# Kernel tuning notes

Hardware: AMD Instinct MI355X
Metric: run time of the kernel (lower is better)

## Reference

```python
import jax, jax.numpy as jnp
import numpy as np

B, N, D, CDIM = 32, 100000, 3, 128


def setup_inputs() -> dict:
    key = jax.random.key(0)
    ks = jax.random.split(key, 24)
    def lin(kw, kb, out_dim, in_dim):
        s = 1.0 / np.sqrt(in_dim)
        W = jax.random.uniform(kw, (out_dim, in_dim), jnp.float32, -s, s)
        b = jax.random.uniform(kb, (out_dim,), jnp.float32, -s, s)
        return W, b
    inp = {}
    inp["t"] = jnp.zeros((1,), jnp.float32)
    inp["x"] = jax.random.normal(ks[0], (B, N, D), jnp.float32)
    inp["c"] = jax.random.normal(ks[1], (B, CDIM), jnp.float32)
    i = 2
    for tag in ("0", "1", "2"):
        W, b = lin(ks[i], ks[i + 1], D, D); i += 2
        Ws, bs = lin(ks[i], ks[i + 1], D, CDIM); i += 2
        Wb, bb = lin(ks[i], ks[i + 1], D, CDIM); i += 2
        inp["W" + tag], inp["b" + tag] = W, b
        inp["Ws" + tag], inp["bs" + tag] = Ws, bs
        inp["Wb" + tag], inp["bb" + tag] = Wb, bb
    return inp


def _block(x, c, W, b, Ws, bs, Wb, bb):
    # FiLM-conditioned linear: fc(x) * sigmoid(fc_scale(c)) + fc_bias(c)
    scale = jax.nn.sigmoid(c @ Ws.T + bs)[:, None, :]  # [B,1,D]
    bias = (c @ Wb.T + bb)[:, None, :]                  # [B,1,D]
    return (x @ W.T + b) * scale + bias                 # [B,N,D]


def reference(t, x, c,
              W0, b0, Ws0, bs0, Wb0, bb0,
              W1, b1, Ws1, bs1, Wb1, bb1,
              W2, b2, Ws2, bs2, Wb2, bb2):
    h = jnp.tanh(_block(x, c, W0, b0, Ws0, bs0, Wb0, bb0))
    h = jnp.tanh(_block(h, c, W1, b1, Ws1, bs1, Wb1, bb1))
    # last four blocks share the fc_2 / fc_scale_2 / fc_bias_2 weights
    for _ in range(4):
        h = jnp.tanh(_block(h, c, W2, b2, Ws2, bs2, Wb2, bb2))
    return h
```

## Files before the change

### kernel.cpp

```cpp
#include <hip/hip_runtime.h>
#include <math.h>

#define NBATCH 32
#define NPTS   100000
#define CD     128
#define PPT    8

#define C2LOG2E 2.8853900817779268f

#if defined(__has_builtin)
#if __has_builtin(__builtin_amdgcn_exp2f)
#define FAST_EXP2(v) __builtin_amdgcn_exp2f(v)
#endif
#endif
#ifndef FAST_EXP2
#define FAST_EXP2(v) __expf((v) * 0.6931471805599453f)
#endif

__device__ __forceinline__ float tanh_pre(float yp) {
    yp = fminf(fmaxf(yp, -30.0f), 30.0f);
    float e = FAST_EXP2(yp);
    float r = __builtin_amdgcn_rcpf(e + 1.0f);
    return fmaf(-2.0f, r, 1.0f);
}

__global__ void film_params_kernel(
    const float* __restrict__ c,
    const float* __restrict__ W0, const float* __restrict__ b0,
    const float* __restrict__ Ws0, const float* __restrict__ bs0,
    const float* __restrict__ Wb0, const float* __restrict__ bb0,
    const float* __restrict__ W1, const float* __restrict__ b1,
    const float* __restrict__ Ws1, const float* __restrict__ bs1,
    const float* __restrict__ Wb1, const float* __restrict__ bb1,
    const float* __restrict__ W2, const float* __restrict__ b2,
    const float* __restrict__ Ws2, const float* __restrict__ bs2,
    const float* __restrict__ Wb2, const float* __restrict__ bb2,
    float* __restrict__ params)
{
    int idx = blockIdx.x * blockDim.x + threadIdx.x;
    if (idx >= NBATCH * 3 * 3) return;
    int d   = idx % 3;
    int tag = (idx / 3) % 3;
    int b   = idx / 9;

    const float* Wt[3]  = {W0, W1, W2};
    const float* bt[3]  = {b0, b1, b2};
    const float* Wst[3] = {Ws0, Ws1, Ws2};
    const float* bst[3] = {bs0, bs1, bs2};
    const float* Wbt[3] = {Wb0, Wb1, Wb2};
    const float* bbt[3] = {bb0, bb1, bb2};

    const float* crow  = c + b * CD;
    const float* wsrow = Wst[tag] + d * CD;
    const float* wbrow = Wbt[tag] + d * CD;
    float sacc = bst[tag][d];
    float bacc = bbt[tag][d];
    for (int k = 0; k < CD; ++k) {
        float cv = crow[k];
        sacc = fmaf(cv, wsrow[k], sacc);
        bacc = fmaf(cv, wbrow[k], bacc);
    }
    float scale = 1.0f / (1.0f + expf(-sacc));
    float cs = C2LOG2E * scale;

    float* o = params + (b * 3 + tag) * 12;
    o[d * 3 + 0] = cs * Wt[tag][d * 3 + 0];
    o[d * 3 + 1] = cs * Wt[tag][d * 3 + 1];
    o[d * 3 + 2] = cs * Wt[tag][d * 3 + 2];
    o[9 + d]     = C2LOG2E * (bt[tag][d] * scale + bacc);
}

__global__ __launch_bounds__(256) void film_main_kernel(
    const float* __restrict__ x, const float* __restrict__ params,
    float* __restrict__ out, int nthreads)
{
    int t = blockIdx.x * blockDim.x + threadIdx.x;
    if (t >= nthreads) return;
    int p0 = t * PPT;
    int b  = p0 / NPTS;

    const float* P = params + b * 36;
    float M0[9], M1[9], M2[9], v0[3], v1[3], v2[3];
#pragma unroll
    for (int i = 0; i < 9; ++i) { M0[i] = P[i]; M1[i] = P[12 + i]; M2[i] = P[24 + i]; }
#pragma unroll
    for (int i = 0; i < 3; ++i) { v0[i] = P[9 + i]; v1[i] = P[21 + i]; v2[i] = P[33 + i]; }

    float a[3 * PPT];
    const float4* xin = (const float4*)(x + (size_t)p0 * 3);
#pragma unroll
    for (int i = 0; i < (3 * PPT) / 4; ++i) ((float4*)a)[i] = xin[i];

#define APPLY(M, v)                                                       \
    {                                                                     \
        float y0 = fmaf(M[0], h0, fmaf(M[1], h1, fmaf(M[2], h2, v[0]))); \
        float y1 = fmaf(M[3], h0, fmaf(M[4], h1, fmaf(M[5], h2, v[1]))); \
        float y2 = fmaf(M[6], h0, fmaf(M[7], h1, fmaf(M[8], h2, v[2]))); \
        h0 = tanh_pre(y0); h1 = tanh_pre(y1); h2 = tanh_pre(y2);         \
    }

#pragma unroll
    for (int p = 0; p < PPT; ++p) {
        float h0 = a[p * 3 + 0], h1 = a[p * 3 + 1], h2 = a[p * 3 + 2];
        APPLY(M0, v0);
        APPLY(M1, v1);
#pragma unroll
        for (int r = 0; r < 4; ++r) { APPLY(M2, v2); }
        a[p * 3 + 0] = h0; a[p * 3 + 1] = h1; a[p * 3 + 2] = h2;
    }
#undef APPLY

    float4* op = (float4*)(out + (size_t)p0 * 3);
#pragma unroll
    for (int i = 0; i < (3 * PPT) / 4; ++i) op[i] = ((float4*)a)[i];
}

extern "C" void kernel_launch(void* const* d_in, const int* in_sizes, int n_in,
                              void* d_out, int out_size, void* d_ws, size_t ws_size,
                              hipStream_t stream)
{
    const float* x = (const float*)d_in[1];
    const float* c = (const float*)d_in[2];
    float* params = (float*)d_ws;

    film_params_kernel<<<dim3(5), dim3(64), 0, stream>>>(
        c,
        (const float*)d_in[3],  (const float*)d_in[4],  (const float*)d_in[5],
        (const float*)d_in[6],  (const float*)d_in[7],  (const float*)d_in[8],
        (const float*)d_in[9],  (const float*)d_in[10], (const float*)d_in[11],
        (const float*)d_in[12], (const float*)d_in[13], (const float*)d_in[14],
        (const float*)d_in[15], (const float*)d_in[16], (const float*)d_in[17],
        (const float*)d_in[18], (const float*)d_in[19], (const float*)d_in[20],
        params);

    int nthreads = (NBATCH * NPTS) / PPT;
    int grid = (nthreads + 255) / 256;
    film_main_kernel<<<dim3(grid), dim3(256), 0, stream>>>(
        x, params, (float*)d_out, nthreads);
}
```

Measured before the change: 150.1 us.

## Fuse FiLM parameter computation into main kernel with per-batch block mapping

```diff
diff --git a/kernel.cpp b/kernel.cpp
--- a/kernel.cpp
+++ b/kernel.cpp
@@ -5,27 +5,21 @@
 #define NPTS   100000
 #define CD     128
 #define PPT    8
+#define TPB    256
+#define THREADS_PER_BATCH (NPTS / PPT)
+#define BLKS_PER_BATCH 49
 
 #define C2LOG2E 2.8853900817779268f
-
-#if defined(__has_builtin)
-#if __has_builtin(__builtin_amdgcn_exp2f)
-#define FAST_EXP2(v) __builtin_amdgcn_exp2f(v)
-#endif
-#endif
-#ifndef FAST_EXP2
-#define FAST_EXP2(v) __expf((v) * 0.6931471805599453f)
-#endif
+#define LOG2E   1.4426950408889634f
 
 __device__ __forceinline__ float tanh_pre(float yp) {
-    yp = fminf(fmaxf(yp, -30.0f), 30.0f);
-    float e = FAST_EXP2(yp);
+    float e = __builtin_amdgcn_exp2f(yp);
     float r = __builtin_amdgcn_rcpf(e + 1.0f);
     return fmaf(-2.0f, r, 1.0f);
 }
 
-__global__ void film_params_kernel(
-    const float* __restrict__ c,
+__global__ __launch_bounds__(TPB) void film_fused_kernel(
+    const float* __restrict__ x, const float* __restrict__ c,
     const float* __restrict__ W0, const float* __restrict__ b0,
     const float* __restrict__ Ws0, const float* __restrict__ bs0,
     const float* __restrict__ Wb0, const float* __restrict__ bb0,
@@ -35,59 +29,88 @@
     const float* __restrict__ W2, const float* __restrict__ b2,
     const float* __restrict__ Ws2, const float* __restrict__ bs2,
     const float* __restrict__ Wb2, const float* __restrict__ bb2,
-    float* __restrict__ params)
+    float* __restrict__ out)
 {
-    int idx = blockIdx.x * blockDim.x + threadIdx.x;
-    if (idx >= NBATCH * 3 * 3) return;
-    int d   = idx % 3;
-    int tag = (idx / 3) % 3;
-    int b   = idx / 9;
+    __shared__ float lds_part[18][8];
+    __shared__ float lds_red[18];
+    __shared__ float lds_params[36];
 
-    const float* Wt[3]  = {W0, W1, W2};
-    const float* bt[3]  = {b0, b1, b2};
-    const float* Wst[3] = {Ws0, Ws1, Ws2};
-    const float* bst[3] = {bs0, bs1, bs2};
-    const float* Wbt[3] = {Wb0, Wb1, Wb2};
-    const float* bbt[3] = {bb0, bb1, bb2};
+    const int tid = threadIdx.x;
+    const int blk = blockIdx.x;
+    const int b = blk / BLKS_PER_BATCH;
+    const int blk_in_b = blk - b * BLKS_PER_BATCH;
 
-    const float* crow  = c + b * CD;
-    const float* wsrow = Wst[tag] + d * CD;
-    const float* wbrow = Wbt[tag] + d * CD;
-    float sacc = bst[tag][d];
-    float bacc = bbt[tag][d];
-    for (int k = 0; k < CD; ++k) {
-        float cv = crow[k];
-        sacc = fmaf(cv, wsrow[k], sacc);
-        bacc = fmaf(cv, wbrow[k], bacc);
+    if (tid < 144) {
+        const int g = tid >> 3, j = tid & 7;
+        const int tag = g / 6;
+        const int r = g - tag * 6;
+        const int d = r >> 1, which = r & 1;
+        const float* Wsel;
+        if (tag == 0)      Wsel = which ? Wb0 : Ws0;
+        else if (tag == 1) Wsel = which ? Wb1 : Ws1;
+        else               Wsel = which ? Wb2 : Ws2;
+        const float4* row4 = (const float4*)(Wsel + d * CD);
+        const float4* c4   = (const float4*)(c + b * CD);
+        float acc = 0.0f;
+#pragma unroll
+        for (int i = 0; i < 4; ++i) {
+            float4 cv = c4[j * 4 + i];
+            float4 wv = row4[j * 4 + i];
+            acc = fmaf(cv.x, wv.x, acc);
+            acc = fmaf(cv.y, wv.y, acc);
+            acc = fmaf(cv.z, wv.z, acc);
+            acc = fmaf(cv.w, wv.w, acc);
+        }
+        lds_part[g][j] = acc;
     }
-    float scale = 1.0f / (1.0f + expf(-sacc));
-    float cs = C2LOG2E * scale;
+    __syncthreads();
+    if (tid < 18) {
+        float s = 0.0f;
+#pragma unroll
+        for (int j = 0; j < 8; ++j) s += lds_part[tid][j];
+        lds_red[tid] = s;
+    }
+    __syncthreads();
+    if (tid < 9) {
+        const int tag = tid / 3, d = tid - tag * 3;
+        const float *Wt, *bt, *bst, *bbt;
+        if (tag == 0)      { Wt = W0; bt = b0; bst = bs0; bbt = bb0; }
+        else if (tag == 1) { Wt = W1; bt = b1; bst = bs1; bbt = bb1; }
+        else               { Wt = W2; bt = b2; bst = bs2; bbt = bb2; }
+        float sacc = lds_red[tag * 6 + d * 2 + 0] + bst[d];
+        float bacc = lds_red[tag * 6 + d * 2 + 1] + bbt[d];
+        float scale = 1.0f / (1.0f + __builtin_amdgcn_exp2f(-sacc * LOG2E));
+        float cs = C2LOG2E * scale;
+        float* o = lds_params + tag * 12;
+        o[d * 3 + 0] = cs * Wt[d * 3 + 0];
+        o[d * 3 + 1] = cs * Wt[d * 3 + 1];
+        o[d * 3 + 2] = cs * Wt[d * 3 + 2];
+        o[9 + d]     = C2LOG2E * fmaf(bt[d], scale, bacc);
+    }
+    __syncthreads();
 
-    float* o = params + (b * 3 + tag) * 12;
-    o[d * 3 + 0] = cs * Wt[tag][d * 3 + 0];
-    o[d * 3 + 1] = cs * Wt[tag][d * 3 + 1];
-    o[d * 3 + 2] = cs * Wt[tag][d * 3 + 2];
-    o[9 + d]     = C2LOG2E * (bt[tag][d] * scale + bacc);
-}
+    float M0[9], M1[9], M2[9], v0[3], v1[3], v2[3];
+    {
+        const float4* P = (const float4*)lds_params;
+        float4 q;
+        q = P[0]; M0[0]=q.x; M0[1]=q.y; M0[2]=q.z; M0[3]=q.w;
+        q = P[1]; M0[4]=q.x; M0[5]=q.y; M0[6]=q.z; M0[7]=q.w;
+        q = P[2]; M0[8]=q.x; v0[0]=q.y; v0[1]=q.z; v0[2]=q.w;
+        q = P[3]; M1[0]=q.x; M1[1]=q.y; M1[2]=q.z; M1[3]=q.w;
+        q = P[4]; M1[4]=q.x; M1[5]=q.y; M1[6]=q.z; M1[7]=q.w;
+        q = P[5]; M1[8]=q.x; v1[0]=q.y; v1[1]=q.z; v1[2]=q.w;
+        q = P[6]; M2[0]=q.x; M2[1]=q.y; M2[2]=q.z; M2[3]=q.w;
+        q = P[7]; M2[4]=q.x; M2[5]=q.y; M2[6]=q.z; M2[7]=q.w;
+        q = P[8]; M2[8]=q.x; v2[0]=q.y; v2[1]=q.z; v2[2]=q.w;
+    }
 
-__global__ __launch_bounds__(256) void film_main_kernel(
-    const float* __restrict__ x, const float* __restrict__ params,
-    float* __restrict__ out, int nthreads)
-{
-    int t = blockIdx.x * blockDim.x + threadIdx.x;
-    if (t >= nthreads) return;
-    int p0 = t * PPT;
-    int b  = p0 / NPTS;
+    const int t_local = blk_in_b * TPB + tid;
+    if (t_local >= THREADS_PER_BATCH) return;
 
-    const float* P = params + b * 36;
-    float M0[9], M1[9], M2[9], v0[3], v1[3], v2[3];
-#pragma unroll
-    for (int i = 0; i < 9; ++i) { M0[i] = P[i]; M1[i] = P[12 + i]; M2[i] = P[24 + i]; }
-#pragma unroll
-    for (int i = 0; i < 3; ++i) { v0[i] = P[9 + i]; v1[i] = P[21 + i]; v2[i] = P[33 + i]; }
+    const size_t p0 = (size_t)b * NPTS + (size_t)t_local * PPT;
 
     float a[3 * PPT];
-    const float4* xin = (const float4*)(x + (size_t)p0 * 3);
+    const float4* xin = (const float4*)(x + p0 * 3);
 #pragma unroll
     for (int i = 0; i < (3 * PPT) / 4; ++i) ((float4*)a)[i] = xin[i];
 
@@ -110,7 +133,7 @@
     }
 #undef APPLY
 
-    float4* op = (float4*)(out + (size_t)p0 * 3);
+    float4* op = (float4*)(out + p0 * 3);
 #pragma unroll
     for (int i = 0; i < (3 * PPT) / 4; ++i) op[i] = ((float4*)a)[i];
 }
@@ -119,22 +142,13 @@
                               void* d_out, int out_size, void* d_ws, size_t ws_size,
                               hipStream_t stream)
 {
-    const float* x = (const float*)d_in[1];
-    const float* c = (const float*)d_in[2];
-    float* params = (float*)d_ws;
-
-    film_params_kernel<<<dim3(5), dim3(64), 0, stream>>>(
-        c,
+    film_fused_kernel<<<dim3(NBATCH * BLKS_PER_BATCH), dim3(TPB), 0, stream>>>(
+        (const float*)d_in[1],  (const float*)d_in[2],
         (const float*)d_in[3],  (const float*)d_in[4],  (const float*)d_in[5],
         (const float*)d_in[6],  (const float*)d_in[7],  (const float*)d_in[8],
         (const float*)d_in[9],  (const float*)d_in[10], (const float*)d_in[11],
         (const float*)d_in[12], (const float*)d_in[13], (const float*)d_in[14],
         (const float*)d_in[15], (const float*)d_in[16], (const float*)d_in[17],
         (const float*)d_in[18], (const float*)d_in[19], (const float*)d_in[20],
-        params);
-
-    int nthreads = (NBATCH * NPTS) / PPT;
-    int grid = (nthreads + 255) / 256;
-    film_main_kernel<<<dim3(grid), dim3(256), 0, stream>>>(
-        x, params, (float*)d_out, nthreads);
+        (float*)d_out);
 }
```

Result: faster. 144.0 us (-4.0%).
